# Optimization experiments

Hardware: AMD Instinct MI355X
Metric: run time of the kernel (lower is better)

The kernel has to match this reference:

```python
import jax, jax.numpy as jnp
import numpy as np

N_NODES = 327680      # 8192 graphs * 40 nodes/graph
N_EDGES = 2621440     # avg degree 8
NODES_PER_GRAPH = 40


def _lin(k, fan_in, fan_out):
    s = 1.0 / np.sqrt(fan_in)
    return jax.random.uniform(k, (fan_in, fan_out), jnp.float32, -s, s)


def setup_inputs() -> dict:
    key = jax.random.key(0)
    ks = jax.random.split(key, 12)
    x = jax.random.normal(ks[0], (N_NODES, 58), jnp.float32)
    edge_index = jax.random.randint(ks[1], (2, N_EDGES), 0, N_NODES, dtype=jnp.int32)
    return {
        "x": x,
        "edge_index": edge_index,
        "W1": _lin(ks[2], 58, 96),  "b1": jnp.zeros((96,), jnp.float32),
        "W2": _lin(ks[3], 96, 48),  "b2": jnp.zeros((48,), jnp.float32),
        "l1_w": _lin(ks[4], 40 * 48, 256), "l1_b": jnp.zeros((256,), jnp.float32),
        "l2_w": _lin(ks[5], 256, 64),      "l2_b": jnp.zeros((64,), jnp.float32),
        "l3_w": _lin(ks[6], 64, 1),        "l3_b": jnp.zeros((1,), jnp.float32),
    }


def gcn_conv(x, src, dst, W, b, n):
    # PyG GCNConv: h = X W; out[i] = sum_{(j->i)} d_j^-1/2 d_i^-1/2 h[j] + b
    h = x @ W                                   # [N, out]
    deg = jnp.zeros((n,), h.dtype).at[dst].add(1.0)
    dinv = jnp.where(deg > 0, jax.lax.rsqrt(deg), 0.0)
    norm = dinv[src] * dinv[dst]                # [E]
    out = jax.ops.segment_sum(h[src] * norm[:, None], dst, num_segments=n)
    return out + b


def reference(x, edge_index, W1, b1, W2, b2, l1_w, l1_b, l2_w, l2_b, l3_w, l3_b):
    n = x.shape[0]
    loop = jnp.arange(n, dtype=edge_index.dtype)        # self-loops (PyG default)
    src = jnp.concatenate([edge_index[0], loop])
    dst = jnp.concatenate([edge_index[1], loop])
    h = jax.nn.relu(gcn_conv(x, src, dst, W1, b1, n))   # dropout is identity in eval
    h = jax.nn.relu(gcn_conv(h, src, dst, W2, b2, n))
    g = h.reshape(n // NODES_PER_GRAPH, NODES_PER_GRAPH * 48)
    g = jax.nn.relu(g @ l1_w + l1_b)
    g = jax.nn.relu(g @ l2_w + l2_b)
    return jax.nn.sigmoid(g @ l3_w + l3_b)              # [B, 1]
```

## Files before the change

### kernel.cpp

```cpp
#include <hip/hip_runtime.h>

#define N_NODES 327680
#define N_EDGES 2621440
#define NGRAPH  8192
#define NB      640
#define BCAPE   4608

typedef unsigned int uint;
typedef unsigned short u16;
typedef __attribute__((ext_vector_type(8))) short s16x8;
typedef __attribute__((ext_vector_type(4))) float f32x4;

__device__ __forceinline__ float bl(uint u){ return __uint_as_float(u << 16); }
__device__ __forceinline__ float bh(uint u){ return __uint_as_float(u & 0xffff0000u); }
__device__ __forceinline__ u16 f2b(float f){
    uint u = __float_as_uint(f);
    u += 0x7fffu + ((u>>16)&1u);
    return (u16)(u>>16);
}
__device__ __forceinline__ uint pk(float a, float b){
    return (uint)f2b(a) | ((uint)f2b(b) << 16);
}


__device__ void tr_tile(const float* __restrict__ in, u16* __restrict__ out,
                        int K, int N, int Kpad, int kb, int nb){
    __shared__ u16 t[64][72];
    for (int i = threadIdx.x; i < 4096; i += 256){
        int k = i >> 6, n = i & 63;
        int gk = kb + k, gn = nb + n;
        float v = (gk < K && gn < N) ? in[(size_t)gk*N + gn] : 0.f;
        t[n][k] = f2b(v);
    }
    __syncthreads();
    for (int i = threadIdx.x; i < 4096; i += 256){
        int n = i >> 6, k = i & 63;
        int gk = kb + k, gn = nb + n;
        if (gn < N && gk < Kpad) out[(size_t)gn*Kpad + gk] = t[n][k];
    }
}

__global__ __launch_bounds__(256) void k_prep(
    const float* __restrict__ W1, const float* __restrict__ W2,
    const float* __restrict__ l1w, const float* __restrict__ l2w,
    u16* __restrict__ w1t, u16* __restrict__ w2t,
    u16* __restrict__ l1wt, u16* __restrict__ l2wt, int* __restrict__ gcur)
{
    int b = blockIdx.x;
    if (b < 120)      tr_tile(l1w, l1wt, 1920, 256, 1920, (b%30)*64, (b/30)*64);
    else if (b < 124) tr_tile(l2w, l2wt, 256,  64,  256,  (b-120)*64, 0);
    else if (b < 126) tr_tile(W1,  w1t,  58,   96,  64,   0, (b-124)*64);
    else if (b < 128) tr_tile(W2,  w2t,  96,   48,  96,   (b-126)*64, 0);
    else {
        for (int i = threadIdx.x; i < NB; i += 256) gcur[i] = 0;
    }
}


__global__ __launch_bounds__(256) void k_partition(
    const int* __restrict__ src, const int* __restrict__ dst,
    int* __restrict__ gcur, uint* __restrict__ staging)
{
    __shared__ int cnt[NB], base_[NB];
    int tid = threadIdx.x;
    for (int i = tid; i < NB; i += 256) cnt[i] = 0;
    __syncthreads();
    int e0 = blockIdx.x*4096;
    int d[16];
    #pragma unroll
    for (int j = 0; j < 16; ++j){
        d[j] = dst[e0 + j*256 + tid];
        atomicAdd(&cnt[d[j] >> 9], 1);
    }
    __syncthreads();
    for (int i = tid; i < NB; i += 256)
        base_[i] = atomicAdd(&gcur[i], cnt[i]);
    __syncthreads();
    for (int i = tid; i < NB; i += 256) cnt[i] = 0;
    __syncthreads();
    #pragma unroll
    for (int j = 0; j < 16; ++j){
        int e = e0 + j*256 + tid;
        int b = d[j] >> 9;
        int r = atomicAdd(&cnt[b], 1);
        staging[(uint)b*BCAPE + base_[b] + r] = (uint)src[e] | ((uint)(d[j] & 511) << 19);
    }
}


__global__ __launch_bounds__(512) void k_bucket(
    const uint* __restrict__ staging, const int* __restrict__ gcur,
    const float* __restrict__ x,
    int* __restrict__ rowst, int* __restrict__ rendg, float* __restrict__ dinvg,
    int* __restrict__ csr, int* __restrict__ perm, uint* __restrict__ xs32)
{
    __shared__ uint sedge[BCAPE];
    __shared__ int deg[512];
    __shared__ int sc[512];
    __shared__ int cur[512];
    __shared__ int dh[64], dbase[64];
    __shared__ float sdinv[512];
    const int b = blockIdx.x;
    const int tid = threadIdx.x;
    const int lo = b*BCAPE;
    int cnt = gcur[b];
    if (cnt > BCAPE) cnt = BCAPE;
    deg[tid] = 0;
    if (tid < 64) dh[tid] = 0;
    __syncthreads();
    for (int t = tid; t < cnt; t += 512){
        uint ed = staging[lo + t];
        sedge[t] = ed;
        atomicAdd(&deg[ed >> 19], 1);
    }
    __syncthreads();
    int d = deg[tid];
    sc[tid] = d;
    __syncthreads();
    for (int o = 1; o < 512; o <<= 1){
        int v = (tid >= o) ? sc[tid-o] : 0;
        __syncthreads();
        sc[tid] += v;
        __syncthreads();
    }
    int incl = sc[tid];
    int excl = incl - d;
    int gnode = b*512 + tid;
    float dv = 1.0f / sqrtf((float)(d + 1));
    rowst[gnode] = lo + excl;
    rendg[gnode] = lo + incl;
    dinvg[gnode] = dv;
    sdinv[tid] = dv;
    cur[tid] = lo + excl;
    int bin = min(d, 63);
    atomicAdd(&dh[bin], 1);
    __syncthreads();
    if (tid == 0){
        int a = 0;
        #pragma unroll
        for (int i = 0; i < 64; ++i){ dbase[i] = a; a += dh[i]; dh[i] = 0; }
    }
    __syncthreads();
    int pos = dbase[bin] + atomicAdd(&dh[bin], 1);
    perm[b*512 + pos] = gnode;
    for (int t = tid; t < cnt; t += 512){
        uint ed = sedge[t];
        int p = atomicAdd(&cur[ed >> 19], 1);
        csr[p] = (int)(ed & 0x7FFFFu);
    }
    const size_t n0 = (size_t)b*512;
    for (int i = tid; i < 512*32; i += 512){
        int n = i >> 5, c = i & 31;
        float dvn = sdinv[n];
        float a = 0.f, bb = 0.f;
        if (c < 29){
            float2 v = *(const float2*)&x[(n0 + n)*58 + 2*c];
            a = v.x * dvn; bb = v.y * dvn;
        }
        xs32[(n0 + n)*32 + c] = pk(a, bb);
    }
}


__global__ __launch_bounds__(256) void k_gather1(
    const int* __restrict__ rs, const int* __restrict__ re,
    const int* __restrict__ csr, const float* __restrict__ dinv,
    const int* __restrict__ perm,
    const uint4* __restrict__ feat4,
    u16* __restrict__ out)
{
    int slot = (blockIdx.x*256 + threadIdx.x) >> 3;
    int c4 = threadIdx.x & 7;
    int node = perm[slot];
    uint4 u = feat4[((uint)node << 3) + c4];
    float a0 = bl(u.x), a1 = bh(u.x), a2 = bl(u.y), a3 = bh(u.y);
    float a4 = bl(u.z), a5 = bh(u.z), a6 = bl(u.w), a7 = bh(u.w);
    int e = rs[node];
    const int e1 = re[node];
    while (e < e1){
        const int last = e1 - 1;
        int idx[8];
        #pragma unroll
        for (int k = 0; k < 8; ++k) idx[k] = csr[min(e + k, last)];
        uint4 uu[8];
        #pragma unroll
        for (int k = 0; k < 8; ++k) uu[k] = feat4[((uint)idx[k] << 3) + c4];
        #pragma unroll
        for (int k = 0; k < 8; ++k){
            if (e + k < e1){
                a0 += bl(uu[k].x); a1 += bh(uu[k].x);
                a2 += bl(uu[k].y); a3 += bh(uu[k].y);
                a4 += bl(uu[k].z); a5 += bh(uu[k].z);
                a6 += bl(uu[k].w); a7 += bh(uu[k].w);
            }
        }
        e += 8;
    }
    float di = dinv[node];
    a0 *= di; a1 *= di; a2 *= di; a3 *= di;
    a4 *= di; a5 *= di; a6 *= di; a7 *= di;
    uint4 w;
    w.x = pk(a0,a1); w.y = pk(a2,a3); w.z = pk(a4,a5); w.w = pk(a6,a7);
    *(uint4*)&out[(size_t)node*64 + c4*8] = w;
}


__global__ __launch_bounds__(256) void k_conv_mlp(
    const u16* __restrict__ A,
    const u16* __restrict__ w1t,
    const float* __restrict__ b1,
    const u16* __restrict__ w2t,
    const float* __restrict__ dinv,
    u16* __restrict__ ts)
{
    __shared__ __align__(16) u16 As[64][72];
    __shared__ __align__(16) u16 Bt1[96][72];
    __shared__ __align__(16) u16 Bt2[48][104];
    __shared__ __align__(16) u16 sh1[64][104];
    __shared__ float sb1[96];
    const int tid = threadIdx.x;
    {
        const u16* Ab = A + (size_t)blockIdx.x*64*64;
        for (int i = tid; i < 512; i += 256){
            int r = i >> 3, s = i & 7;
            *(uint4*)&As[r][s*8] = *(const uint4*)&Ab[r*64 + s*8];
        }
    }
    for (int i = tid; i < 768; i += 256){
        int n = i >> 3, s = i & 7;
        *(uint4*)&Bt1[n][s*8] = *(const uint4*)&w1t[n*64 + s*8];
    }
    for (int i = tid; i < 576; i += 256){
        int n = i / 12, s = i % 12;
        *(uint4*)&Bt2[n][s*8] = *(const uint4*)&w2t[n*96 + s*8];
    }
    if (tid < 96) sb1[tid] = b1[tid];
    __syncthreads();

    const int wv = tid >> 6, l = tid & 63;
    const int lr = l & 15, lg = l >> 4;
    const int r0 = wv*16;

    f32x4 acc1[6] = {};
    #pragma unroll
    for (int s = 0; s < 2; ++s){
        s16x8 af = *(const s16x8*)&As[r0+lr][s*32 + lg*8];
        #pragma unroll
        for (int t = 0; t < 6; ++t){
            s16x8 bf = *(const s16x8*)&Bt1[t*16+lr][s*32 + lg*8];
            acc1[t] = __builtin_amdgcn_mfma_f32_16x16x32_bf16(af, bf, acc1[t], 0, 0, 0);
        }
    }
    #pragma unroll
    for (int t = 0; t < 6; ++t){
        int col = t*16 + lr;
        float bias = sb1[col];
        #pragma unroll
        for (int r = 0; r < 4; ++r)
            sh1[r0 + lg*4 + r][col] = f2b(fmaxf(acc1[t][r] + bias, 0.f));
    }
    __syncthreads();

    f32x4 acc2[3] = {};
    #pragma unroll
    for (int s = 0; s < 3; ++s){
        s16x8 af = *(const s16x8*)&sh1[r0+lr][s*32 + lg*8];
        #pragma unroll
        for (int t = 0; t < 3; ++t){
            s16x8 bf = *(const s16x8*)&Bt2[t*16+lr][s*32 + lg*8];
            acc2[t] = __builtin_amdgcn_mfma_f32_16x16x32_bf16(af, bf, acc2[t], 0, 0, 0);
        }
    }
    size_t gbase = (size_t)blockIdx.x*64;
    #pragma unroll
    for (int r = 0; r < 4; ++r){
        size_t row = gbase + r0 + lg*4 + r;
        float dv = dinv[row];
        #pragma unroll
        for (int t = 0; t < 3; ++t)
            ts[row*64 + t*16 + lr] = f2b(acc2[t][r] * dv);
        ts[row*64 + 48 + lr] = 0;
    }
}


__global__ __launch_bounds__(256) void k_gather2(
    const int* __restrict__ rs, const int* __restrict__ re,
    const int* __restrict__ csr, const float* __restrict__ dinv,
    const int* __restrict__ perm,
    const uint4* __restrict__ feat4,
    const float* __restrict__ bias,
    u16* __restrict__ out)
{
    int slot = (blockIdx.x*256 + threadIdx.x) >> 3;
    int c4 = threadIdx.x & 7;
    int node = perm[slot];
    uint4 u = feat4[((uint)node << 3) + c4];
    float a0 = bl(u.x), a1 = bh(u.x), a2 = bl(u.y), a3 = bh(u.y);
    float a4 = bl(u.z), a5 = bh(u.z), a6 = bl(u.w), a7 = bh(u.w);
    int e = rs[node];
    const int e1 = re[node];
    while (e < e1){
        const int last = e1 - 1;
        int idx[8];
        #pragma unroll
        for (int k = 0; k < 8; ++k) idx[k] = csr[min(e + k, last)];
        uint4 uu[8];
        #pragma unroll
        for (int k = 0; k < 8; ++k) uu[k] = feat4[((uint)idx[k] << 3) + c4];
        #pragma unroll
        for (int k = 0; k < 8; ++k){
            if (e + k < e1){
                a0 += bl(uu[k].x); a1 += bh(uu[k].x);
                a2 += bl(uu[k].y); a3 += bh(uu[k].y);
                a4 += bl(uu[k].z); a5 += bh(uu[k].z);
                a6 += bl(uu[k].w); a7 += bh(uu[k].w);
            }
        }
        e += 8;
    }
    float di = dinv[node];
    if (c4 < 6){
        float4 bz0 = *(const float4*)&bias[8*c4];
        float4 bz1 = *(const float4*)&bias[8*c4 + 4];
        a0 = fmaxf(a0*di + bz0.x, 0.f); a1 = fmaxf(a1*di + bz0.y, 0.f);
        a2 = fmaxf(a2*di + bz0.z, 0.f); a3 = fmaxf(a3*di + bz0.w, 0.f);
        a4 = fmaxf(a4*di + bz1.x, 0.f); a5 = fmaxf(a5*di + bz1.y, 0.f);
        a6 = fmaxf(a6*di + bz1.z, 0.f); a7 = fmaxf(a7*di + bz1.w, 0.f);
        uint4 w;
        w.x = pk(a0,a1); w.y = pk(a2,a3); w.z = pk(a4,a5); w.w = pk(a6,a7);
        *(uint4*)&out[(size_t)node*48 + c4*8] = w;
    }
}


__global__ __launch_bounds__(256) void k_head(
    const u16* __restrict__ A,
    const u16* __restrict__ l1wt,
    const float* __restrict__ l1b,
    const u16* __restrict__ l2wt,
    const float* __restrict__ l2b,
    const float* __restrict__ l3w, const float* __restrict__ l3b,
    float* __restrict__ out)
{
    __shared__ __align__(16) u16 As[32][72];
    __shared__ __align__(16) u16 Bt[256][72];
    __shared__ float part[32][2];
    u16 (*sh1)[264] = (u16(*)[264])&Bt[0][0];
    const int tid = threadIdx.x;
    const int g0 = blockIdx.x*32;
    const int w = tid >> 6, l = tid & 63;
    const int lr = l & 15, lg = l >> 4;
    const int r0 = (w & 1)*16;
    const int c0 = (w >> 1)*128;
    f32x4 acc[8] = {};
    for (int k0 = 0; k0 < 1920; k0 += 64){
        __syncthreads();
        {
            int r = tid >> 3, s = tid & 7;
            *(uint4*)&As[r][s*8] = *(const uint4*)&A[(size_t)(g0+r)*1920 + k0 + s*8];
        }
        for (int i = tid; i < 2048; i += 256){
            int n = i >> 3, s = i & 7;
            *(uint4*)&Bt[n][s*8] = *(const uint4*)&l1wt[(size_t)n*1920 + k0 + s*8];
        }
        __syncthreads();
        #pragma unroll
        for (int s = 0; s < 2; ++s){
            s16x8 af = *(const s16x8*)&As[r0+lr][s*32 + lg*8];
            #pragma unroll
            for (int t = 0; t < 8; ++t){
                s16x8 bf = *(const s16x8*)&Bt[c0 + t*16 + lr][s*32 + lg*8];
                acc[t] = __builtin_amdgcn_mfma_f32_16x16x32_bf16(af, bf, acc[t], 0, 0, 0);
            }
        }
    }
    __syncthreads();
    #pragma unroll
    for (int t = 0; t < 8; ++t){
        int col = c0 + t*16 + lr;
        float bs = l1b[col];
        #pragma unroll
        for (int r = 0; r < 4; ++r)
            sh1[r0 + lg*4 + r][col] = f2b(fmaxf(acc[t][r] + bs, 0.f));
    }
    __syncthreads();
    f32x4 acc2[2] = {};
    #pragma unroll
    for (int s = 0; s < 8; ++s){
        s16x8 af = *(const s16x8*)&sh1[r0+lr][s*32 + lg*8];
        #pragma unroll
        for (int t = 0; t < 2; ++t){
            int col = (w>>1)*32 + t*16 + lr;
            s16x8 bf = *(const s16x8*)&l2wt[(size_t)col*256 + s*32 + lg*8];
            acc2[t] = __builtin_amdgcn_mfma_f32_16x16x32_bf16(af, bf, acc2[t], 0, 0, 0);
        }
    }
    float p[4];
    #pragma unroll
    for (int r = 0; r < 4; ++r){
        p[r] = 0.f;
        #pragma unroll
        for (int t = 0; t < 2; ++t){
            int col = (w>>1)*32 + t*16 + lr;
            p[r] += fmaxf(acc2[t][r] + l2b[col], 0.f) * l3w[col];
        }
    }
    #pragma unroll
    for (int o = 1; o < 16; o <<= 1){
        #pragma unroll
        for (int r = 0; r < 4; ++r) p[r] += __shfl_xor(p[r], o);
    }
    if (lr == 0){
        #pragma unroll
        for (int r = 0; r < 4; ++r)
            part[r0 + lg*4 + r][w>>1] = p[r];
    }
    __syncthreads();
    if (tid < 32)
        out[g0 + tid] = 1.0f / (1.0f + expf(-(part[tid][0] + part[tid][1] + l3b[0])));
}

extern "C" void kernel_launch(void* const* d_in, const int* in_sizes, int n_in,
                              void* d_out, int out_size, void* d_ws, size_t ws_size,
                              hipStream_t stream){
    const float* x   = (const float*)d_in[0];
    const int*   ei  = (const int*)  d_in[1];
    const int*   src = ei;
    const int*   dst = ei + N_EDGES;
    const float* W1  = (const float*)d_in[2];
    const float* b1  = (const float*)d_in[3];
    const float* W2  = (const float*)d_in[4];
    const float* b2  = (const float*)d_in[5];
    const float* l1w = (const float*)d_in[6];
    const float* l1b = (const float*)d_in[7];
    const float* l2w = (const float*)d_in[8];
    const float* l2b = (const float*)d_in[9];
    const float* l3w = (const float*)d_in[10];
    const float* l3b = (const float*)d_in[11];
    float* out = (float*)d_out;

    char* w = (char*)d_ws;
    auto alloc = [&](size_t bytes){ void* p = (void*)w; w += (bytes + 255) & ~(size_t)255; return p; };
    float* dinv    = (float*)alloc((size_t)N_NODES*4);
    int*   rowst   = (int*)  alloc((size_t)N_NODES*4);
    int*   rend    = (int*)  alloc((size_t)N_NODES*4);
    int*   perm    = (int*)  alloc((size_t)N_NODES*4);
    int*   gcur    = (int*)  alloc(NB*4);
    u16*   w1t     = (u16*)  alloc(96*64*2);
    u16*   w2t     = (u16*)  alloc(48*96*2);
    u16*   l1wt    = (u16*)  alloc((size_t)256*1920*2);
    u16*   l2wt    = (u16*)  alloc((size_t)64*256*2);
    int*   csr     = (int*)  alloc((size_t)NB*BCAPE*4);
    uint*  staging = (uint*) alloc((size_t)NB*BCAPE*4);
    char*  BUF_P   = (char*) alloc((size_t)N_NODES*32*4);
    char*  BUF_Q   = (char*) alloc((size_t)N_NODES*64*2);

    uint* xs32 = (uint*)BUF_P;
    u16*  ts   = (u16*) BUF_P;
    u16*  agg1 = (u16*) BUF_Q;
    u16*  agg2 = (u16*) BUF_Q;

    k_prep     <<<129, 256, 0, stream>>>(W1, W2, l1w, l2w, w1t, w2t, l1wt, l2wt, gcur);

    k_partition<<<640, 256, 0, stream>>>(src, dst, gcur, staging);
    k_bucket   <<<640, 512, 0, stream>>>(staging, gcur, x, rowst, rend, dinv, csr, perm, xs32);

    k_gather1  <<<10240, 256, 0, stream>>>(rowst, rend, csr, dinv, perm,
                                           (const uint4*)xs32, agg1);
    k_conv_mlp <<<5120,  256, 0, stream>>>(agg1, w1t, b1, w2t, dinv, ts);

    k_gather2  <<<10240, 256, 0, stream>>>(rowst, rend, csr, dinv, perm,
                                           (const uint4*)ts, b2, agg2);

    k_head     <<<256, 256, 0, stream>>>(agg2, l1wt, l1b, l2wt, l2b, l3w, l3b, out);
}
```

Baseline: 339.4 us.

## Use wave-shuffle scan in bucket kernel and widen conv_mlp and head blocks to 512 threads

Replaces the shared-memory Hillis-Steele prefix scan in k_bucket with a wavefront __shfl_up scan plus a small cross-wave combine, which removes many block barriers. k_conv_mlp now processes 128 rows per 512-thread block so the weight tiles are loaded once for twice as many rows. k_head uses 8 waves instead of 4, splitting the l1 output columns and l2 columns across more waves to use more of the GPU, since it launches only 256 blocks. The cost is more shared memory per conv_mlp block, which may lower occupancy, and more partial-sum reduction work in the head.

```diff
diff --git a/kernel.cpp b/kernel.cpp
--- a/kernel.cpp
+++ b/kernel.cpp
@@ -96,8 +96,8 @@
 {
     __shared__ uint sedge[BCAPE];
     __shared__ int deg[512];
-    __shared__ int sc[512];
     __shared__ int cur[512];
+    __shared__ int wsum[8];
     __shared__ int dh[64], dbase[64];
     __shared__ float sdinv[512];
     const int b = blockIdx.x;
@@ -115,15 +115,21 @@
     }
     __syncthreads();
     int d = deg[tid];
-    sc[tid] = d;
-    __syncthreads();
-    for (int o = 1; o < 512; o <<= 1){
-        int v = (tid >= o) ? sc[tid-o] : 0;
-        __syncthreads();
-        sc[tid] += v;
-        __syncthreads();
-    }
-    int incl = sc[tid];
+    int incl = d;
+    #pragma unroll
+    for (int o = 1; o < 64; o <<= 1){
+        int t = __shfl_up(incl, o);
+        if ((tid & 63) >= o) incl += t;
+    }
+    if ((tid & 63) == 63) wsum[tid >> 6] = incl;
+    __syncthreads();
+    if (tid == 0){
+        int a = 0;
+        #pragma unroll
+        for (int i = 0; i < 8; ++i){ int v = wsum[i]; wsum[i] = a; a += v; }
+    }
+    __syncthreads();
+    incl += wsum[tid >> 6];
     int excl = incl - d;
     int gnode = b*512 + tid;
     float dv = 1.0f / sqrtf((float)(d + 1));
@@ -205,7 +211,7 @@
 }
 
 
-__global__ __launch_bounds__(256) void k_conv_mlp(
+__global__ __launch_bounds__(512) void k_conv_mlp(
     const u16* __restrict__ A,
     const u16* __restrict__ w1t,
     const float* __restrict__ b1,
@@ -213,24 +219,24 @@
     const float* __restrict__ dinv,
     u16* __restrict__ ts)
 {
-    __shared__ __align__(16) u16 As[64][72];
+    __shared__ __align__(16) u16 As[128][72];
     __shared__ __align__(16) u16 Bt1[96][72];
     __shared__ __align__(16) u16 Bt2[48][104];
-    __shared__ __align__(16) u16 sh1[64][104];
+    __shared__ __align__(16) u16 sh1[128][104];
     __shared__ float sb1[96];
     const int tid = threadIdx.x;
     {
-        const u16* Ab = A + (size_t)blockIdx.x*64*64;
-        for (int i = tid; i < 512; i += 256){
+        const u16* Ab = A + (size_t)blockIdx.x*128*64;
+        for (int i = tid; i < 1024; i += 512){
             int r = i >> 3, s = i & 7;
             *(uint4*)&As[r][s*8] = *(const uint4*)&Ab[r*64 + s*8];
         }
     }
-    for (int i = tid; i < 768; i += 256){
+    for (int i = tid; i < 768; i += 512){
         int n = i >> 3, s = i & 7;
         *(uint4*)&Bt1[n][s*8] = *(const uint4*)&w1t[n*64 + s*8];
     }
-    for (int i = tid; i < 576; i += 256){
+    for (int i = tid; i < 576; i += 512){
         int n = i / 12, s = i % 12;
         *(uint4*)&Bt2[n][s*8] = *(const uint4*)&w2t[n*96 + s*8];
     }
@@ -271,7 +277,7 @@
             acc2[t] = __builtin_amdgcn_mfma_f32_16x16x32_bf16(af, bf, acc2[t], 0, 0, 0);
         }
     }
-    size_t gbase = (size_t)blockIdx.x*64;
+    size_t gbase = (size_t)blockIdx.x*128;
     #pragma unroll
     for (int r = 0; r < 4; ++r){
         size_t row = gbase + r0 + lg*4 + r;
@@ -334,7 +340,7 @@
 }
 
 
-__global__ __launch_bounds__(256) void k_head(
+__global__ __launch_bounds__(512) void k_head(
     const u16* __restrict__ A,
     const u16* __restrict__ l1wt,
     const float* __restrict__ l1b,
@@ -345,22 +351,22 @@
 {
     __shared__ __align__(16) u16 As[32][72];
     __shared__ __align__(16) u16 Bt[256][72];
-    __shared__ float part[32][2];
+    __shared__ float part[32][4];
     u16 (*sh1)[264] = (u16(*)[264])&Bt[0][0];
     const int tid = threadIdx.x;
     const int g0 = blockIdx.x*32;
     const int w = tid >> 6, l = tid & 63;
     const int lr = l & 15, lg = l >> 4;
     const int r0 = (w & 1)*16;
-    const int c0 = (w >> 1)*128;
-    f32x4 acc[8] = {};
+    const int c0 = (w >> 1)*64;
+    f32x4 acc[4] = {};
     for (int k0 = 0; k0 < 1920; k0 += 64){
         __syncthreads();
-        {
+        if (tid < 256){
             int r = tid >> 3, s = tid & 7;
             *(uint4*)&As[r][s*8] = *(const uint4*)&A[(size_t)(g0+r)*1920 + k0 + s*8];
         }
-        for (int i = tid; i < 2048; i += 256){
+        for (int i = tid; i < 2048; i += 512){
             int n = i >> 3, s = i & 7;
             *(uint4*)&Bt[n][s*8] = *(const uint4*)&l1wt[(size_t)n*1920 + k0 + s*8];
         }
@@ -369,7 +375,7 @@
         for (int s = 0; s < 2; ++s){
             s16x8 af = *(const s16x8*)&As[r0+lr][s*32 + lg*8];
             #pragma unroll
-            for (int t = 0; t < 8; ++t){
+            for (int t = 0; t < 4; ++t){
                 s16x8 bf = *(const s16x8*)&Bt[c0 + t*16 + lr][s*32 + lg*8];
                 acc[t] = __builtin_amdgcn_mfma_f32_16x16x32_bf16(af, bf, acc[t], 0, 0, 0);
             }
@@ -377,7 +383,7 @@
     }
     __syncthreads();
     #pragma unroll
-    for (int t = 0; t < 8; ++t){
+    for (int t = 0; t < 4; ++t){
         int col = c0 + t*16 + lr;
         float bs = l1b[col];
         #pragma unroll
@@ -385,27 +391,19 @@
             sh1[r0 + lg*4 + r][col] = f2b(fmaxf(acc[t][r] + bs, 0.f));
     }
     __syncthreads();
-    f32x4 acc2[2] = {};
+    f32x4 acc2 = {};
+    const int col = (w >> 1)*16 + lr;
     #pragma unroll
     for (int s = 0; s < 8; ++s){
         s16x8 af = *(const s16x8*)&sh1[r0+lr][s*32 + lg*8];
-        #pragma unroll
-        for (int t = 0; t < 2; ++t){
-            int col = (w>>1)*32 + t*16 + lr;
-            s16x8 bf = *(const s16x8*)&l2wt[(size_t)col*256 + s*32 + lg*8];
-            acc2[t] = __builtin_amdgcn_mfma_f32_16x16x32_bf16(af, bf, acc2[t], 0, 0, 0);
-        }
-    }
+        s16x8 bf = *(const s16x8*)&l2wt[(size_t)col*256 + s*32 + lg*8];
+        acc2 = __builtin_amdgcn_mfma_f32_16x16x32_bf16(af, bf, acc2, 0, 0, 0);
+    }
+    float lb = l2b[col], lw = l3w[col];
     float p[4];
     #pragma unroll
-    for (int r = 0; r < 4; ++r){
-        p[r] = 0.f;
-        #pragma unroll
-        for (int t = 0; t < 2; ++t){
-            int col = (w>>1)*32 + t*16 + lr;
-            p[r] += fmaxf(acc2[t][r] + l2b[col], 0.f) * l3w[col];
-        }
-    }
+    for (int r = 0; r < 4; ++r)
+        p[r] = fmaxf(acc2[r] + lb, 0.f) * lw;
     #pragma unroll
     for (int o = 1; o < 16; o <<= 1){
         #pragma unroll
@@ -418,7 +416,8 @@
     }
     __syncthreads();
     if (tid < 32)
-        out[g0 + tid] = 1.0f / (1.0f + expf(-(part[tid][0] + part[tid][1] + l3b[0])));
+        out[g0 + tid] = 1.0f / (1.0f + expf(-(part[tid][0] + part[tid][1]
+                                            + part[tid][2] + part[tid][3] + l3b[0])));
 }
 
 extern "C" void kernel_launch(void* const* d_in, const int* in_sizes, int n_in,
@@ -468,10 +467,10 @@
 
     k_gather1  <<<10240, 256, 0, stream>>>(rowst, rend, csr, dinv, perm,
                                            (const uint4*)xs32, agg1);
-    k_conv_mlp <<<5120,  256, 0, stream>>>(agg1, w1t, b1, w2t, dinv, ts);
+    k_conv_mlp <<<2560,  512, 0, stream>>>(agg1, w1t, b1, w2t, dinv, ts);
 
     k_gather2  <<<10240, 256, 0, stream>>>(rowst, rend, csr, dinv, perm,
                                            (const uint4*)ts, b2, agg2);
 
-    k_head     <<<256, 256, 0, stream>>>(agg2, l1wt, l1b, l2wt, l2b, l3w, l3b, out);
-}
+    k_head     <<<256, 512, 0, stream>>>(agg2, l1wt, l1b, l2wt, l2b, l3w, l3b, out);
+}
```

New measurement: 337.3 us. About the same (-0.6%).
